# Performance work log

Measured on AMD Instinct MI355X. Metric: run time of the kernel, lower is better.

## Reference

```python
import jax, jax.numpy as jnp
import numpy as np

N_NODES = 100000


def gcn_layer(x, edge_index, W, b):
    """PyG GCNConv: h = D^-1/2 (A+I) D^-1/2 (x W) + b, scatter-sum aggregation."""
    n = x.shape[0]
    h = x @ W  # [N, out]
    loop = jnp.arange(n, dtype=edge_index.dtype)
    src = jnp.concatenate([edge_index[0], loop])  # [E+N]
    dst = jnp.concatenate([edge_index[1], loop])
    deg = jax.ops.segment_sum(jnp.ones_like(dst, dtype=h.dtype), dst, num_segments=n)
    dinv = jnp.where(deg > 0, jax.lax.rsqrt(deg), 0.0)
    norm = dinv[src] * dinv[dst]  # [E+N]
    msg = h[src] * norm[:, None]  # gather + scale (largest intermediate)
    out = jax.ops.segment_sum(msg, dst, num_segments=n)
    return out + b


def setup_inputs() -> dict:
    key = jax.random.key(0)
    k = jax.random.split(key, 8)
    in_dim, hid_dim, out_dim = 128, 64, 112
    E = 1600000
    x = jax.random.normal(k[0], (N_NODES, in_dim), dtype=jnp.float32)
    edge_index = jax.random.randint(k[1], (2, E), 0, N_NODES, dtype=jnp.int32)
    s1 = 1.0 / np.sqrt(in_dim)
    s2 = 1.0 / np.sqrt(hid_dim)
    return {
        "x": x,
        "edge_index": edge_index,
        "W1": jax.random.uniform(k[2], (in_dim, hid_dim), jnp.float32, -s1, s1),
        "b1": jnp.zeros((hid_dim,), jnp.float32),
        "W2": jax.random.uniform(k[3], (hid_dim, hid_dim), jnp.float32, -s2, s2),
        "b2": jnp.zeros((hid_dim,), jnp.float32),
        "W3": jax.random.uniform(k[4], (hid_dim, out_dim), jnp.float32, -s2, s2),
        "b3": jnp.zeros((out_dim,), jnp.float32),
    }


def reference(x, edge_index, W1, b1, W2, b2, W3, b3):
    # eval mode: dropout is identity
    h = jax.nn.relu(gcn_layer(x, edge_index, W1, b1))
    h = jax.nn.relu(gcn_layer(h, edge_index, W2, b2))
    return gcn_layer(h, edge_index, W3, b3)
```

## Files before the change

kernel.cpp:

```cpp
#include <hip/hip_runtime.h>
#include <hip/hip_fp16.h>
#include <math.h>


#define IN_DIM 128
#define HID 64
#define OUT_DIM 112
#define LSHIFT 7
#define LMASK 127
#define MAXBUCK 1024
#define CHUNK 8192
#define CAP 4096

typedef _Float16 f16x8 __attribute__((ext_vector_type(8)));
typedef float f32x4 __attribute__((ext_vector_type(4)));

template <int K, int C>
__device__ __forceinline__ void stage_w(const float* __restrict__ W, _Float16* Wt) {
  constexpr int KP = K + 8;
  for (int idx = threadIdx.x; idx < K * C; idx += 256) {
    int k = idx / C, c = idx % C;
    Wt[c * KP + k] = (_Float16)W[idx];
  }
}

template <int K, int C, bool XH, bool DINV, bool BIAS, bool OUTH>
__device__ __forceinline__ void gemm_compute(int blk, const void* __restrict__ Xv,
                                             const float* __restrict__ dinv,
                                             const float* __restrict__ bias,
                                             void* __restrict__ G, int n,
                                             const _Float16* Wt) {
  constexpr int KP = K + 8;
  constexpr int NT = C / 16;
  constexpr int KS = K / 32;
  const int tid = threadIdx.x;
  const int l = tid & 63;
  const int rbase = blk * 64 + (tid >> 6) * 16;
  const int kg = (l >> 4) * 8;
  const int c16 = l & 15;

  int arow = rbase + c16;
  if (arow >= n) arow = n - 1;
  f16x8 af[KS];
  if (XH) {
    const _Float16* Xh = reinterpret_cast<const _Float16*>(Xv);
#pragma unroll
    for (int ks = 0; ks < KS; ++ks)
      af[ks] = *reinterpret_cast<const f16x8*>(&Xh[(size_t)arow * K + ks * 32 + kg]);
  } else {
    const float* Xf = reinterpret_cast<const float*>(Xv);
#pragma unroll
    for (int ks = 0; ks < KS; ++ks) {
      float4 u0 = *reinterpret_cast<const float4*>(&Xf[(size_t)arow * K + ks * 32 + kg]);
      float4 u1 = *reinterpret_cast<const float4*>(&Xf[(size_t)arow * K + ks * 32 + kg + 4]);
      f16x8 a;
      a[0] = (_Float16)u0.x; a[1] = (_Float16)u0.y; a[2] = (_Float16)u0.z; a[3] = (_Float16)u0.w;
      a[4] = (_Float16)u1.x; a[5] = (_Float16)u1.y; a[6] = (_Float16)u1.z; a[7] = (_Float16)u1.w;
      af[ks] = a;
    }
  }

  f32x4 acc[NT];
#pragma unroll
  for (int nt = 0; nt < NT; ++nt) acc[nt] = (f32x4){0.f, 0.f, 0.f, 0.f};

#pragma unroll
  for (int ks = 0; ks < KS; ++ks) {
#pragma unroll
    for (int nt = 0; nt < NT; ++nt) {
      f16x8 bf = *reinterpret_cast<const f16x8*>(&Wt[(nt * 16 + c16) * KP + ks * 32 + kg]);
      acc[nt] = __builtin_amdgcn_mfma_f32_16x16x32_f16(af[ks], bf, acc[nt], 0, 0, 0);
    }
  }

#pragma unroll
  for (int r = 0; r < 4; ++r) {
    int grow = rbase + (l >> 4) * 4 + r;
    if (grow < n) {
      float s = DINV ? dinv[grow] : 1.0f;
#pragma unroll
      for (int nt = 0; nt < NT; ++nt) {
        float v = acc[nt][r] * s;
        if (BIAS) v += bias[nt * 16 + c16];
        if (OUTH)
          reinterpret_cast<__half*>(G)[(size_t)grow * C + nt * 16 + c16] = __float2half(v);
        else
          reinterpret_cast<float*>(G)[(size_t)grow * C + nt * 16 + c16] = v;
      }
    }
  }
}

template <bool RELU, bool BIAS, bool TSCALE>
__device__ __forceinline__ void agg_item(int grp, const __half* __restrict__ g,
                                         const int* __restrict__ row_start,
                                         const int* __restrict__ ssrc,
                                         const float* __restrict__ dinv,
                                         const float* __restrict__ bias,
                                         __half* __restrict__ out, int n) {
  const int tid = threadIdx.x;
  const int wv = tid >> 6;
  const int lane = tid & 63;
  const int h = lane >> 5;
  const int q = lane & 31;
  const int node = grp * 4 + wv;
  if (node < n) {
    const __half2* g2 = reinterpret_cast<const __half2*>(g);
    int e0 = row_start[node];
    int e1 = row_start[node + 1];
    int deg = e1 - e0;
    float2 acc = make_float2(0.f, 0.f);
    if (h == 0) {
      float2 sv = __half22float2(g2[(size_t)node * 32 + q]);
      acc.x = sv.x; acc.y = sv.y;
    }
    const int pairs = deg >> 1;
    const int base = e0 + h;
    int k = 0;
    for (; k + 8 <= pairs; k += 8) {
      int idx[8];
#pragma unroll
      for (int i = 0; i < 8; ++i) idx[i] = ssrc[base + 2 * (k + i)];
      __half2 v[8];
#pragma unroll
      for (int i = 0; i < 8; ++i) v[i] = g2[(size_t)idx[i] * 32 + q];
#pragma unroll
      for (int i = 0; i < 8; ++i) {
        float2 f = __half22float2(v[i]);
        acc.x += f.x; acc.y += f.y;
      }
    }
    for (; k + 2 <= pairs; k += 2) {
      int i0 = ssrc[base + 2 * k];
      int i1 = ssrc[base + 2 * (k + 1)];
      float2 f0 = __half22float2(g2[(size_t)i0 * 32 + q]);
      float2 f1 = __half22float2(g2[(size_t)i1 * 32 + q]);
      acc.x += f0.x + f1.x; acc.y += f0.y + f1.y;
    }
    for (; k < pairs; ++k) {
      int i0 = ssrc[base + 2 * k];
      float2 f = __half22float2(g2[(size_t)i0 * 32 + q]);
      acc.x += f.x; acc.y += f.y;
    }
    if ((deg & 1) && h == 0) {
      int i0 = ssrc[e1 - 1];
      float2 f = __half22float2(g2[(size_t)i0 * 32 + q]);
      acc.x += f.x; acc.y += f.y;
    }
    acc.x += __shfl_xor(acc.x, 32);
    acc.y += __shfl_xor(acc.y, 32);

    if (h == 0) {
      float di = dinv[node];
      float rx = acc.x * di, ry = acc.y * di;
      if (BIAS) {
        float2 bv = *reinterpret_cast<const float2*>(&bias[2 * q]);
        rx += bv.x; ry += bv.y;
      }
      if (RELU) { rx = fmaxf(rx, 0.f); ry = fmaxf(ry, 0.f); }
      if (TSCALE) { rx *= di; ry *= di; }
      reinterpret_cast<__half2*>(out)[(size_t)node * 32 + q] = __floats2half2_rn(rx, ry);
    }
  }
}

__global__ __launch_bounds__(256) void gemm1_hist_kernel(
    const float* __restrict__ x, const float* __restrict__ W1, __half* __restrict__ gh,
    int n, const int* __restrict__ dst, int* __restrict__ H,
    int E, int nbuck, int nchunk) {
  __shared__ __align__(16) char smem[HID * (IN_DIM + 8) * 2];
  const int tid = threadIdx.x;
  if ((int)blockIdx.x < nchunk) {
    int* hist = reinterpret_cast<int*>(smem);
    for (int i = tid; i < nbuck; i += 256) hist[i] = 0;
    __syncthreads();
    int lo = blockIdx.x * CHUNK, hi = min(E, lo + CHUNK);
    for (int i = lo + tid; i < hi; i += 256)
      atomicAdd(&hist[dst[i] >> LSHIFT], 1);
    __syncthreads();
    int* Hrow = &H[(size_t)blockIdx.x * nbuck];
    for (int i = tid; i < nbuck; i += 256) Hrow[i] = hist[i];
  } else {
    _Float16* Wt = reinterpret_cast<_Float16*>(smem);
    stage_w<IN_DIM, HID>(W1, Wt);
    __syncthreads();
    gemm_compute<IN_DIM, HID, false, false, false, true>(
        (int)blockIdx.x - nchunk, x, nullptr, nullptr, gh, n, Wt);
  }
}

__global__ __launch_bounds__(256) void chunk_prefix_kernel(int* __restrict__ H,
                                                           int* __restrict__ cb,
                                                           int nchunk, int nbuck) {
  int wv = threadIdx.x >> 6, lane = threadIdx.x & 63;
  int b = blockIdx.x * 4 + wv;
  if (b >= nbuck) return;
  int run = 0;
  for (int c0 = 0; c0 < nchunk; c0 += 64) {
    int c = c0 + lane;
    int v = (c < nchunk) ? H[(size_t)c * nbuck + b] : 0;
    int incl = v;
#pragma unroll
    for (int off = 1; off < 64; off <<= 1) {
      int u = __shfl_up(incl, off);
      if (lane >= off) incl += u;
    }
    if (c < nchunk) H[(size_t)c * nbuck + b] = run + incl - v;
    run += __shfl(incl, 63);
  }
  if (lane == 0) cb[b] = run;
}

__global__ __launch_bounds__(256) void coarse_scatter_kernel(
    const int* __restrict__ src, const int* __restrict__ dst,
    const int* __restrict__ H, int* __restrict__ packed, int E, int nbuck) {
  __shared__ int cur[MAXBUCK];
  const int tid = threadIdx.x;
  const int* Hrow = &H[(size_t)blockIdx.x * nbuck];
  for (int i = tid; i < nbuck; i += 256) cur[i] = Hrow[i];
  __syncthreads();
  int lo = blockIdx.x * CHUNK, hi = min(E, lo + CHUNK);
  for (int i = lo + tid; i < hi; i += 256) {
    int s = src[i], d = dst[i];
    int b = d >> LSHIFT;
    int off = atomicAdd(&cur[b], 1);
    if (off < CAP) packed[(size_t)b * CAP + off] = (s << LSHIFT) | (d & LMASK);
  }
}

__global__ __launch_bounds__(256) void fine_fused_kernel(
    const int* __restrict__ packed, const int* __restrict__ cb,
    int* __restrict__ row_start, float* __restrict__ dinv,
    int* __restrict__ ssrc, __half* __restrict__ gh, int n, int nbuck) {
  const int b = blockIdx.x;
  const int t = threadIdx.x;
  __shared__ int hist[128];
  __shared__ int pfx[128];
  __shared__ int cur[128];
  __shared__ float sdi[128];
  __shared__ int red[4];
  __shared__ int sbase;
  if (t < 128) hist[t] = 0;
  __syncthreads();
  const int cbb = min(cb[b], CAP);
  const int* pk = &packed[(size_t)b * CAP];
  for (int e = t; e < cbb; e += 256) atomicAdd(&hist[pk[e] & LMASK], 1);
  int partial = 0;
  for (int i = t; i < b; i += 256) partial += min(cb[i], CAP);
#pragma unroll
  for (int off = 1; off < 64; off <<= 1) partial += __shfl_xor(partial, off);
  const int lane = t & 63, wv = t >> 6;
  if (lane == 0) red[wv] = partial;
  __syncthreads();
  if (t == 0) sbase = red[0] + red[1] + red[2] + red[3];
  if (t < 128) pfx[t] = hist[t];
  __syncthreads();
  for (int off = 1; off < 128; off <<= 1) {
    int u = (t >= off && t < 128) ? pfx[t - off] : 0;
    __syncthreads();
    if (t < 128) pfx[t] += u;
    __syncthreads();
  }
  if (t < 128) {
    int node = b * 128 + t;
    if (node < n) {
      int rs = sbase + pfx[t] - hist[t];
      row_start[node] = rs;
      float di = 1.0f / sqrtf((float)(hist[t] + 1));
      dinv[node] = di;
      sdi[t] = di;
      cur[t] = rs;
    } else {
      sdi[t] = 0.f;
      cur[t] = 0;
    }
  }
  if (b == nbuck - 1 && t == 0) row_start[n] = sbase + cbb;
  __syncthreads();
  for (int e = t; e < cbb; e += 256) {
    int p = pk[e];
    int slot = atomicAdd(&cur[p & LMASK], 1);
    ssrc[slot] = p >> LSHIFT;
  }
  __half2* g2 = reinterpret_cast<__half2*>(gh);
  for (int i = t; i < 128 * 32; i += 256) {
    int nd = i >> 5;
    int node = b * 128 + nd;
    if (node < n) {
      int q = i & 31;
      float2 f = __half22float2(g2[(size_t)node * 32 + q]);
      float d = sdi[nd];
      g2[(size_t)node * 32 + q] = __floats2half2_rn(f.x * d, f.y * d);
    }
  }
}

template <bool RELU, bool BIAS, bool TSCALE>
__global__ __launch_bounds__(256) void agg_kernel(const __half* __restrict__ g,
                                                  const int* __restrict__ row_start,
                                                  const int* __restrict__ ssrc,
                                                  const float* __restrict__ dinv,
                                                  const float* __restrict__ bias,
                                                  __half* __restrict__ out, int n) {
  agg_item<RELU, BIAS, TSCALE>(blockIdx.x, g, row_start, ssrc, dinv, bias, out, n);
}

__global__ __launch_bounds__(256) void agg1_gemm2_kernel(
    const __half* __restrict__ gh, const int* __restrict__ row_start,
    const int* __restrict__ ssrc, const float* __restrict__ dinv,
    const float* __restrict__ b1, __half* __restrict__ h1h,
    const float* __restrict__ W2, __half* __restrict__ g2h, int n) {
  __shared__ _Float16 Wt[HID * (HID + 8)];
  stage_w<HID, HID>(W2, Wt);
  const int blk = blockIdx.x;
#pragma unroll 1
  for (int i = 0; i < 16; ++i)
    agg_item<true, true, false>(blk * 16 + i, gh, row_start, ssrc, dinv, b1, h1h, n);
  __syncthreads();
  gemm_compute<HID, HID, true, true, false, true>(blk, h1h, dinv, nullptr, g2h, n, Wt);
}

__global__ __launch_bounds__(256) void agg3_gemm3_kernel(
    const __half* __restrict__ th, const int* __restrict__ row_start,
    const int* __restrict__ ssrc, const float* __restrict__ dinv,
    __half* __restrict__ h1h, const float* __restrict__ W3,
    const float* __restrict__ b3, float* __restrict__ out, int n) {
  __shared__ _Float16 Wt[OUT_DIM * (HID + 8)];
  stage_w<HID, OUT_DIM>(W3, Wt);
  const int blk = blockIdx.x;
#pragma unroll 1
  for (int i = 0; i < 16; ++i)
    agg_item<false, false, false>(blk * 16 + i, th, row_start, ssrc, dinv, nullptr, h1h, n);
  __syncthreads();
  gemm_compute<HID, OUT_DIM, true, false, true, false>(blk, h1h, nullptr, b3, out, n, Wt);
}

extern "C" void kernel_launch(void* const* d_in, const int* in_sizes, int n_in,
                              void* d_out, int out_size, void* d_ws, size_t ws_size,
                              hipStream_t stream) {
  const float* x = (const float*)d_in[0];
  const int* ei = (const int*)d_in[1];
  const float* W1 = (const float*)d_in[2];
  const float* b1 = (const float*)d_in[3];
  const float* W2 = (const float*)d_in[4];
  const float* b2 = (const float*)d_in[5];
  const float* W3 = (const float*)d_in[6];
  const float* b3 = (const float*)d_in[7];
  float* out = (float*)d_out;

  const int n = in_sizes[0] / IN_DIM;
  const int E = in_sizes[1] / 2;
  const int* src = ei;
  const int* dst = ei + E;
  const int nbuck = (n + LMASK) >> LSHIFT;
  const int nchunk = (E + CHUNK - 1) / CHUNK;

  char* p = (char*)d_ws;
  auto alloc = [&](size_t bytes) {
    char* q = p;
    p += (bytes + 255) & ~(size_t)255;
    return q;
  };
  float* dinv = (float*)alloc((size_t)n * 4);
  int* row_start = (int*)alloc((size_t)(n + 1) * 4);
  int* H = (int*)alloc((size_t)nchunk * nbuck * 4);
  int* cb = (int*)alloc((size_t)(nbuck + 1) * 4);
  int* packed = (int*)alloc((size_t)nbuck * CAP * 4);
  int* ssrc = (int*)alloc((size_t)E * 4);
  __half* gh  = (__half*)alloc((size_t)n * HID * 2);
  __half* h1h = (__half*)alloc((size_t)n * HID * 2);
  __half* g2h = (__half*)alloc((size_t)n * HID * 2);
  __half* th  = (__half*)alloc((size_t)n * HID * 2);

  const int GG = (n + 63) / 64;

  gemm1_hist_kernel<<<nchunk + GG, 256, 0, stream>>>(x, W1, gh, n, dst, H, E, nbuck, nchunk);
  chunk_prefix_kernel<<<(nbuck + 3) / 4, 256, 0, stream>>>(H, cb, nchunk, nbuck);
  coarse_scatter_kernel<<<nchunk, 256, 0, stream>>>(src, dst, H, packed, E, nbuck);
  fine_fused_kernel<<<nbuck, 256, 0, stream>>>(packed, cb, row_start, dinv, ssrc, gh, n, nbuck);
  agg1_gemm2_kernel<<<GG, 256, 0, stream>>>(gh, row_start, ssrc, dinv, b1, h1h, W2, g2h, n);
  agg_kernel<true, true, true><<<(n + 3) / 4, 256, 0, stream>>>(g2h, row_start, ssrc, dinv, b2, th, n);
  agg3_gemm3_kernel<<<GG, 256, 0, stream>>>(th, row_start, ssrc, dinv, h1h, W3, b3, out, n);
}
```

Before: 392.2 us.

## Split fused aggregation+GEMM kernels into separate aggregation and MFMA GEMM launches

Result: faster. 352.6 us (-10.1%).

```diff
diff --git a/kernel.cpp b/kernel.cpp
--- a/kernel.cpp
+++ b/kernel.cpp
@@ -91,77 +91,16 @@
   }
 }
 
-template <bool RELU, bool BIAS, bool TSCALE>
-__device__ __forceinline__ void agg_item(int grp, const __half* __restrict__ g,
-                                         const int* __restrict__ row_start,
-                                         const int* __restrict__ ssrc,
-                                         const float* __restrict__ dinv,
-                                         const float* __restrict__ bias,
-                                         __half* __restrict__ out, int n) {
-  const int tid = threadIdx.x;
-  const int wv = tid >> 6;
-  const int lane = tid & 63;
-  const int h = lane >> 5;
-  const int q = lane & 31;
-  const int node = grp * 4 + wv;
-  if (node < n) {
-    const __half2* g2 = reinterpret_cast<const __half2*>(g);
-    int e0 = row_start[node];
-    int e1 = row_start[node + 1];
-    int deg = e1 - e0;
-    float2 acc = make_float2(0.f, 0.f);
-    if (h == 0) {
-      float2 sv = __half22float2(g2[(size_t)node * 32 + q]);
-      acc.x = sv.x; acc.y = sv.y;
-    }
-    const int pairs = deg >> 1;
-    const int base = e0 + h;
-    int k = 0;
-    for (; k + 8 <= pairs; k += 8) {
-      int idx[8];
-#pragma unroll
-      for (int i = 0; i < 8; ++i) idx[i] = ssrc[base + 2 * (k + i)];
-      __half2 v[8];
-#pragma unroll
-      for (int i = 0; i < 8; ++i) v[i] = g2[(size_t)idx[i] * 32 + q];
-#pragma unroll
-      for (int i = 0; i < 8; ++i) {
-        float2 f = __half22float2(v[i]);
-        acc.x += f.x; acc.y += f.y;
-      }
-    }
-    for (; k + 2 <= pairs; k += 2) {
-      int i0 = ssrc[base + 2 * k];
-      int i1 = ssrc[base + 2 * (k + 1)];
-      float2 f0 = __half22float2(g2[(size_t)i0 * 32 + q]);
-      float2 f1 = __half22float2(g2[(size_t)i1 * 32 + q]);
-      acc.x += f0.x + f1.x; acc.y += f0.y + f1.y;
-    }
-    for (; k < pairs; ++k) {
-      int i0 = ssrc[base + 2 * k];
-      float2 f = __half22float2(g2[(size_t)i0 * 32 + q]);
-      acc.x += f.x; acc.y += f.y;
-    }
-    if ((deg & 1) && h == 0) {
-      int i0 = ssrc[e1 - 1];
-      float2 f = __half22float2(g2[(size_t)i0 * 32 + q]);
-      acc.x += f.x; acc.y += f.y;
-    }
-    acc.x += __shfl_xor(acc.x, 32);
-    acc.y += __shfl_xor(acc.y, 32);
-
-    if (h == 0) {
-      float di = dinv[node];
-      float rx = acc.x * di, ry = acc.y * di;
-      if (BIAS) {
-        float2 bv = *reinterpret_cast<const float2*>(&bias[2 * q]);
-        rx += bv.x; ry += bv.y;
-      }
-      if (RELU) { rx = fmaxf(rx, 0.f); ry = fmaxf(ry, 0.f); }
-      if (TSCALE) { rx *= di; ry *= di; }
-      reinterpret_cast<__half2*>(out)[(size_t)node * 32 + q] = __floats2half2_rn(rx, ry);
-    }
-  }
+template <int K, int C, bool XH, bool DINV, bool BIAS, bool OUTH>
+__global__ __launch_bounds__(256) void mfma_gemm_kernel(const void* __restrict__ Xv,
+                                                        const float* __restrict__ W,
+                                                        const float* __restrict__ dinv,
+                                                        const float* __restrict__ bias,
+                                                        void* __restrict__ G, int n) {
+  __shared__ _Float16 Wt[C * (K + 8)];
+  stage_w<K, C>(W, Wt);
+  __syncthreads();
+  gemm_compute<K, C, XH, DINV, BIAS, OUTH>(blockIdx.x, Xv, dinv, bias, G, n, Wt);
 }
 
 __global__ __launch_bounds__(256) void gemm1_hist_kernel(
@@ -302,37 +241,70 @@
                                                   const float* __restrict__ dinv,
                                                   const float* __restrict__ bias,
                                                   __half* __restrict__ out, int n) {
-  agg_item<RELU, BIAS, TSCALE>(blockIdx.x, g, row_start, ssrc, dinv, bias, out, n);
-}
-
-__global__ __launch_bounds__(256) void agg1_gemm2_kernel(
-    const __half* __restrict__ gh, const int* __restrict__ row_start,
-    const int* __restrict__ ssrc, const float* __restrict__ dinv,
-    const float* __restrict__ b1, __half* __restrict__ h1h,
-    const float* __restrict__ W2, __half* __restrict__ g2h, int n) {
-  __shared__ _Float16 Wt[HID * (HID + 8)];
-  stage_w<HID, HID>(W2, Wt);
-  const int blk = blockIdx.x;
-#pragma unroll 1
-  for (int i = 0; i < 16; ++i)
-    agg_item<true, true, false>(blk * 16 + i, gh, row_start, ssrc, dinv, b1, h1h, n);
-  __syncthreads();
-  gemm_compute<HID, HID, true, true, false, true>(blk, h1h, dinv, nullptr, g2h, n, Wt);
-}
-
-__global__ __launch_bounds__(256) void agg3_gemm3_kernel(
-    const __half* __restrict__ th, const int* __restrict__ row_start,
-    const int* __restrict__ ssrc, const float* __restrict__ dinv,
-    __half* __restrict__ h1h, const float* __restrict__ W3,
-    const float* __restrict__ b3, float* __restrict__ out, int n) {
-  __shared__ _Float16 Wt[OUT_DIM * (HID + 8)];
-  stage_w<HID, OUT_DIM>(W3, Wt);
-  const int blk = blockIdx.x;
-#pragma unroll 1
-  for (int i = 0; i < 16; ++i)
-    agg_item<false, false, false>(blk * 16 + i, th, row_start, ssrc, dinv, nullptr, h1h, n);
-  __syncthreads();
-  gemm_compute<HID, OUT_DIM, true, false, true, false>(blk, h1h, nullptr, b3, out, n, Wt);
+  const int tid = threadIdx.x;
+  const int wv = tid >> 6;
+  const int lane = tid & 63;
+  const int h = lane >> 5;
+  const int q = lane & 31;
+  int node = blockIdx.x * 4 + wv;
+  if (node >= n) return;
+  const __half2* g2 = reinterpret_cast<const __half2*>(g);
+
+  int e0 = row_start[node];
+  int e1 = row_start[node + 1];
+  int deg = e1 - e0;
+  float2 acc = make_float2(0.f, 0.f);
+  if (h == 0) {
+    float2 sv = __half22float2(g2[(size_t)node * 32 + q]);
+    acc.x = sv.x; acc.y = sv.y;
+  }
+  const int pairs = deg >> 1;
+  const int base = e0 + h;
+  int k = 0;
+  for (; k + 8 <= pairs; k += 8) {
+    int idx[8];
+#pragma unroll
+    for (int i = 0; i < 8; ++i) idx[i] = ssrc[base + 2 * (k + i)];
+    __half2 v[8];
+#pragma unroll
+    for (int i = 0; i < 8; ++i) v[i] = g2[(size_t)idx[i] * 32 + q];
+#pragma unroll
+    for (int i = 0; i < 8; ++i) {
+      float2 f = __half22float2(v[i]);
+      acc.x += f.x; acc.y += f.y;
+    }
+  }
+  for (; k + 2 <= pairs; k += 2) {
+    int i0 = ssrc[base + 2 * k];
+    int i1 = ssrc[base + 2 * (k + 1)];
+    float2 f0 = __half22float2(g2[(size_t)i0 * 32 + q]);
+    float2 f1 = __half22float2(g2[(size_t)i1 * 32 + q]);
+    acc.x += f0.x + f1.x; acc.y += f0.y + f1.y;
+  }
+  for (; k < pairs; ++k) {
+    int i0 = ssrc[base + 2 * k];
+    float2 f = __half22float2(g2[(size_t)i0 * 32 + q]);
+    acc.x += f.x; acc.y += f.y;
+  }
+  if ((deg & 1) && h == 0) {
+    int i0 = ssrc[e1 - 1];
+    float2 f = __half22float2(g2[(size_t)i0 * 32 + q]);
+    acc.x += f.x; acc.y += f.y;
+  }
+  acc.x += __shfl_xor(acc.x, 32);
+  acc.y += __shfl_xor(acc.y, 32);
+
+  if (h == 0) {
+    float di = dinv[node];
+    float rx = acc.x * di, ry = acc.y * di;
+    if (BIAS) {
+      float2 bv = *reinterpret_cast<const float2*>(&bias[2 * q]);
+      rx += bv.x; ry += bv.y;
+    }
+    if (RELU) { rx = fmaxf(rx, 0.f); ry = fmaxf(ry, 0.f); }
+    if (TSCALE) { rx *= di; ry *= di; }
+    reinterpret_cast<__half2*>(out)[(size_t)node * 32 + q] = __floats2half2_rn(rx, ry);
+  }
 }
 
 extern "C" void kernel_launch(void* const* d_in, const int* in_sizes, int n_in,
@@ -369,16 +341,21 @@
   int* ssrc = (int*)alloc((size_t)E * 4);
   __half* gh  = (__half*)alloc((size_t)n * HID * 2);
   __half* h1h = (__half*)alloc((size_t)n * HID * 2);
-  __half* g2h = (__half*)alloc((size_t)n * HID * 2);
   __half* th  = (__half*)alloc((size_t)n * HID * 2);
 
   const int GG = (n + 63) / 64;
+  const int AGRID = (n + 3) / 4;
 
   gemm1_hist_kernel<<<nchunk + GG, 256, 0, stream>>>(x, W1, gh, n, dst, H, E, nbuck, nchunk);
   chunk_prefix_kernel<<<(nbuck + 3) / 4, 256, 0, stream>>>(H, cb, nchunk, nbuck);
   coarse_scatter_kernel<<<nchunk, 256, 0, stream>>>(src, dst, H, packed, E, nbuck);
   fine_fused_kernel<<<nbuck, 256, 0, stream>>>(packed, cb, row_start, dinv, ssrc, gh, n, nbuck);
-  agg1_gemm2_kernel<<<GG, 256, 0, stream>>>(gh, row_start, ssrc, dinv, b1, h1h, W2, g2h, n);
-  agg_kernel<true, true, true><<<(n + 3) / 4, 256, 0, stream>>>(g2h, row_start, ssrc, dinv, b2, th, n);
-  agg3_gemm3_kernel<<<GG, 256, 0, stream>>>(th, row_start, ssrc, dinv, h1h, W3, b3, out, n);
-}
+
+  agg_kernel<true, true, false><<<AGRID, 256, 0, stream>>>(gh, row_start, ssrc, dinv, b1, h1h, n);
+
+  mfma_gemm_kernel<HID, HID, true, true, false, true><<<GG, 256, 0, stream>>>(h1h, W2, dinv, nullptr, gh, n);
+  agg_kernel<true, true, true><<<AGRID, 256, 0, stream>>>(gh, row_start, ssrc, dinv, b2, th, n);
+
+  agg_kernel<false, false, false><<<AGRID, 256, 0, stream>>>(th, row_start, ssrc, dinv, nullptr, h1h, n);
+  mfma_gemm_kernel<HID, OUT_DIM, true, false, true, false><<<GG, 256, 0, stream>>>(h1h, W3, nullptr, b3, out, n);
+}
```
